# Optimization experiments

Measured on AMD Instinct MI355X. Metric: run time of the kernel, lower is better.

## Reference

```python
import jax, jax.numpy as jnp
import numpy as np

B, S, D, H = 4, 2048, 512, 8
DEPTH = D // H


def setup_inputs() -> dict:
    key = jax.random.key(0)
    ks = jax.random.split(key, 12)
    scale = 0.02
    inp = {
        "q": jax.random.normal(ks[0], (B, S, D), dtype=jnp.float32),
        "k": jax.random.normal(ks[1], (B, S, D), dtype=jnp.float32),
        "v": jax.random.normal(ks[2], (B, S, D), dtype=jnp.float32),
        "mask": jax.random.randint(ks[3], (B, S, S), 0, 2, dtype=jnp.int32),
        "wq": jax.random.normal(ks[4], (D, D), dtype=jnp.float32) * scale,
        "bq": jnp.zeros((D,), dtype=jnp.float32),
        "wk": jax.random.normal(ks[5], (D, D), dtype=jnp.float32) * scale,
        "bk": jnp.zeros((D,), dtype=jnp.float32),
        "wv": jax.random.normal(ks[6], (D, D), dtype=jnp.float32) * scale,
        "bv": jnp.zeros((D,), dtype=jnp.float32),
        "wo": jax.random.normal(ks[7], (D, D), dtype=jnp.float32) * scale,
        "bo": jnp.zeros((D,), dtype=jnp.float32),
    }
    return inp


def _split_heads(x):
    # [B, S, D] -> [B, H, S, depth]
    b, s, _ = x.shape
    return x.reshape(b, s, H, DEPTH).transpose(0, 2, 1, 3)


def reference(q, k, v, mask, wq, bq, wk, bk, wv, bv, wo, bo):
    qh = _split_heads(q @ wq + bq)
    kh = _split_heads(k @ wk + bk)
    vh = _split_heads(v @ wv + bv)
    # scaled dot-product attention with additive mask, materializing [B,H,S,S]
    scores = jnp.einsum("bhqd,bhkd->bhqk", qh, kh) / jnp.sqrt(
        jnp.asarray(DEPTH, jnp.float32)
    )
    scores = scores + mask[:, None, :, :].astype(jnp.float32) * (-1e9)
    w = jax.nn.softmax(scores, axis=-1)
    o = jnp.einsum("bhqk,bhkd->bhqd", w, vh)
    o = o.transpose(0, 2, 1, 3).reshape(q.shape[0], -1, D)  # [B, S, D]
    return o @ wo + bo
```

## Files before the change

kernel.cpp:

```cpp
#include <hip/hip_runtime.h>
#include <hip/hip_bf16.h>
#include <stdint.h>

#define B_ 4
#define S_ 2048
#define D_ 512
#define H_ 8

typedef __attribute__((ext_vector_type(8))) short short8;
typedef __attribute__((ext_vector_type(4))) short short4v;
typedef __attribute__((ext_vector_type(4))) float f32x4;
typedef __attribute__((ext_vector_type(4))) unsigned short u16x4;

#define MFMA16(a,b,c) __builtin_amdgcn_mfma_f32_16x16x32_bf16((a),(b),(c),0,0,0)

#if __has_builtin(__builtin_amdgcn_mfma_f32_16x16x16bf16_1k)
#define HAVE16K 1
#define MFMA16K(a,b,c) __builtin_amdgcn_mfma_f32_16x16x16bf16_1k((a),(b),(c),0,0,0)
#else
#define HAVE16K 0
#endif

#if __has_builtin(__builtin_amdgcn_sbfe)
#define SBFE1(v, off) ((uint32_t)__builtin_amdgcn_sbfe((int)(v), (off), 1))
#else
#define SBFE1(v, off) ((uint32_t)(((int32_t)((v) << (31-(off)))) >> 31))
#endif

__device__ __forceinline__ unsigned short f2bf(float f){
    return __builtin_bit_cast(unsigned short, __float2bfloat16(f));
}

__device__ __forceinline__ float maskf(float p, uint32_t keep){
    return __builtin_bit_cast(float, __builtin_bit_cast(uint32_t, p) & keep);
}

__device__ __forceinline__ float max3f(float a, float b, float c){
    float d;
    asm("v_max3_f32 %0, %1, %2, %3" : "=v"(d) : "v"(a), "v"(b), "v"(c));
    return d;
}

__device__ __forceinline__ void gload_lds16(const void* g, void* l){
    __builtin_amdgcn_global_load_lds((const __attribute__((address_space(1))) uint32_t*)g,
                                     (__attribute__((address_space(3))) uint32_t*)l, 16, 0, 0);
}

__global__ __launch_bounds__(256) void maskpack_kernel(const int* __restrict__ mask,
                                                       uint32_t* __restrict__ out)
{
    int idx = blockIdx.x*256 + threadIdx.x;
    const int4* p = (const int4*)(mask + (size_t)idx*32);
    uint32_t bits = 0;
    #pragma unroll
    for (int c=0;c<8;c++){
        int4 v = p[c];
        if (v.x) bits |= 1u << (c*4+0);
        if (v.y) bits |= 1u << (c*4+1);
        if (v.z) bits |= 1u << (c*4+2);
        if (v.w) bits |= 1u << (c*4+3);
    }
    out[idx] = bits;
}

__global__ __launch_bounds__(256) void wtrans_kernel(const float* __restrict__ wq,
                                                     const float* __restrict__ wk,
                                                     const float* __restrict__ wv,
                                                     const float* __restrict__ wo,
                                                     unsigned short* __restrict__ wt)
{
    int f = blockIdx.x*256 + threadIdx.x;
    int mat = f >> 18;
    int rem = f & 262143;
    const float* Wm = (mat==0)?wq:(mat==1)?wk:(mat==2)?wv:wo;
    int kk = rem >> 9, nn = rem & 511;
    wt[(size_t)mat*262144 + (size_t)nn*512 + kk] = f2bf(Wm[rem]);
}

__global__ __launch_bounds__(256) void proj_kernel(
    const float* __restrict__ q, const float* __restrict__ k, const float* __restrict__ v,
    const float* __restrict__ bq, const float* __restrict__ bk, const float* __restrict__ bv,
    const unsigned short* __restrict__ wt, unsigned short* __restrict__ outb)
{
    __shared__ uint8_t smem[16384];
    const int t = threadIdx.x, l = t&63, w = t>>6, g = l>>4, ln = l&15;
    const int z = blockIdx.z;
    const float* X = (z==0)? q : (z==1)? k : v;
    const float* bias = (z==0)? bq : (z==1)? bk : bv;
    const unsigned short* WTz = wt + (size_t)z*(D_*D_);
    unsigned short* out = outb + (size_t)z*((size_t)B_*H_*S_*64);
    const float scale = (z==0)? 0.18033688011112042f : 1.0f;
    const int m0 = blockIdx.x*128, n0 = blockIdx.y*128;
    uint8_t* As = smem; uint8_t* Bs = smem + 8192;
    const int RB = (w>>1)*64, CB = (w&1)*64;

    const f32x4 zz = {0.f,0.f,0.f,0.f};
    f32x4 acc[4][4];
    #pragma unroll
    for (int i=0;i<4;i++)
        #pragma unroll
        for (int j=0;j<4;j++) acc[i][j] = zz;

    for (int k0=0; k0<D_; k0+=32){
        __syncthreads();
        #pragma unroll
        for (int i=0;i<2;i++){
            int qc = w + i*4;
            int row = qc*16 + (l>>2);
            int colb = ((l&3)*16) ^ ((row&3)<<4);
            gload_lds16((const uint8_t*)WTz + (((size_t)(n0+row)*D_ + k0)<<1) + colb,
                        Bs + qc*1024);
        }
        #pragma unroll
        for (int i=0;i<2;i++){
            int c = t + i*256;
            int row = c>>2, cc = c&3;
            const float4* src = (const float4*)(X + (size_t)(m0+row)*D_ + k0 + cc*8);
            float4 u0 = src[0], u1 = src[1];
            uint32_t c0,c1,c2,c3;
            asm("v_cvt_pk_bf16_f32 %0, %1, %2" : "=v"(c0) : "v"(u0.x), "v"(u0.y));
            asm("v_cvt_pk_bf16_f32 %0, %1, %2" : "=v"(c1) : "v"(u0.z), "v"(u0.w));
            asm("v_cvt_pk_bf16_f32 %0, %1, %2" : "=v"(c2) : "v"(u1.x), "v"(u1.y));
            asm("v_cvt_pk_bf16_f32 %0, %1, %2" : "=v"(c3) : "v"(u1.z), "v"(u1.w));
            uint4 pk4; pk4.x=c0; pk4.y=c1; pk4.z=c2; pk4.w=c3;
            *(uint4*)(As + row*64 + ((cc*16) ^ ((row&3)<<4))) = pk4;
        }
        __syncthreads();
        short8 af[4], bfr[4];
        #pragma unroll
        for (int ai=0; ai<4; ai++){
            int row = RB + 16*ai + ln;
            af[ai] = *(const short8*)(As + row*64 + ((16*g) ^ ((row&3)<<4)));
        }
        #pragma unroll
        for (int bj=0; bj<4; bj++){
            int row = CB + 16*bj + ln;
            bfr[bj] = *(const short8*)(Bs + row*64 + ((16*g) ^ ((row&3)<<4)));
        }
        if (z == 2){
            #pragma unroll
            for (int ai=0; ai<4; ai++)
                #pragma unroll
                for (int bj=0; bj<4; bj++)
                    acc[ai][bj] = MFMA16(bfr[bj], af[ai], acc[ai][bj]);
        } else {
            #pragma unroll
            for (int ai=0; ai<4; ai++)
                #pragma unroll
                for (int bj=0; bj<4; bj++)
                    acc[ai][bj] = MFMA16(af[ai], bfr[bj], acc[ai][bj]);
        }
    }

    if (z == 2){
        #pragma unroll
        for (int bj=0; bj<4; bj++){
            #pragma unroll
            for (int ai=0; ai<4; ai++){
                int s = m0 + RB + 16*ai + ln;
                #pragma unroll
                for (int r=0;r<4;r++){
                    int gn = n0 + CB + 16*bj + 4*g + r;
                    float val = acc[ai][bj][r] + bias[gn];
                    out[((size_t)(s>>11)*D_ + gn)*S_ + (s&2047)] = f2bf(val);
                }
            }
        }
    } else {
        #pragma unroll
        for (int bj=0; bj<4; bj++){
            int gn = n0 + CB + 16*bj + ln;
            float bv2 = bias[gn];
            int h = gn >> 6, dep = gn & 63;
            #pragma unroll
            for (int ai=0; ai<4; ai++){
                #pragma unroll
                for (int r=0;r<4;r++){
                    int gm = m0 + RB + 16*ai + 4*g + r;
                    float val = (acc[ai][bj][r] + bv2) * scale;
                    size_t o = ((size_t)(gm>>11)*H_ + h)*((size_t)S_*64) + (size_t)(gm&2047)*64 + dep;
                    out[o] = f2bf(val);
                }
            }
        }
    }
}

__global__ __launch_bounds__(256, 4) void attn_kernel(
    const unsigned short* __restrict__ qb, const unsigned short* __restrict__ kb,
    const unsigned short* __restrict__ vtb, const uint32_t* __restrict__ mb,
    unsigned short* __restrict__ ao)
{
#if HAVE16K
    __shared__ uint8_t smem[32768];
#else
    __shared__ uint8_t smem[40960];
#endif
    const int t = threadIdx.x, l = t&63, w = t>>6, g = l>>4, ln = l&15;
    const int bh = blockIdx.y;
    const int b = bh >> 3;
    const int q0 = blockIdx.x * 64;
    const unsigned short* Q  = qb + (size_t)bh*((size_t)S_*64);
    const unsigned short* K  = kb + (size_t)bh*((size_t)S_*64);
    const unsigned short* VT = vtb + ((size_t)b*D_ + (bh&7)*64)*S_;

    const int qrow = q0 + 16*w + ln;
    const short8 qf0 = *(const short8*)(Q + (size_t)qrow*64 + 8*g);
    const short8 qf1 = *(const short8*)(Q + (size_t)qrow*64 + 8*g + 32);

    const int Msw = (ln&7)<<4;
    const int sw0 = (16*g) ^ Msw;
    const int sw1 = (16*g + 64) ^ Msw;
    uint8_t* kB0 = smem + ln*128 + sw0;
    uint8_t* kB1 = smem + ln*128 + sw1;
#if HAVE16K
    uint8_t* vB  = smem + 16384 + ln*128;
    const int vo0 = (8*g     ) ^ Msw;
    const int vo1 = (8*g + 32) ^ Msw;
    const int vo2 = (8*g + 64) ^ Msw;
    const int vo3 = (8*g + 96) ^ Msw;
#else
    uint8_t* Pw = smem + 32768 + w*2048;
    uint8_t* prd0 = Pw + ln*128 + sw0;
    uint8_t* prd1 = Pw + ln*128 + sw1;
#endif

    int krow0 = w*8 + (l>>3), krow1 = (w+4)*8 + (l>>3);
    int colb0 = ((l&7)*16) ^ ((krow0&7)<<4);
    int colb1 = ((l&7)*16) ^ ((krow1&7)<<4);
    int kof0 = krow0*128 + colb0,     kof1 = krow1*128 + colb1;
    int vof0 = krow0*(S_*2) + colb0,  vof1 = krow1*(S_*2) + colb1;
    const int ldo0 = w*1024, ldo1 = (w+4)*1024;

    const uint2* mptr = (const uint2*)(mb + ((size_t)b*S_ + qrow)*64);

    const f32x4 zz = {0.f,0.f,0.f,0.f};
    f32x4 O[4], O5 = zz;
    #pragma unroll
    for (int i=0;i<4;i++) O[i] = zz;
    float c = 0.f;

    const short4v onesv = {0x3F80,0x3F80,0x3F80,0x3F80};
#if !HAVE16K
    const short8 ones8 = {0x3F80,0x3F80,0x3F80,0x3F80,0x3F80,0x3F80,0x3F80,0x3F80};
#endif

    gload_lds16((const uint8_t*)K  + kof0, smem + ldo0);
    gload_lds16((const uint8_t*)K  + kof1, smem + ldo1);
    gload_lds16((const uint8_t*)VT + vof0, smem + 16384 + ldo0);
    gload_lds16((const uint8_t*)VT + vof1, smem + 16384 + ldo1);
    kof0 += 8192; kof1 += 8192; vof0 += 128; vof1 += 128;
    int curb = 0;
    uint2 mmc = mptr[0];

    for (int it=0; it<S_/64; ++it){
        __syncthreads();
        if (it < S_/64 - 1){
            int nx = curb ^ 8192;
            gload_lds16((const uint8_t*)K  + kof0, smem + nx + ldo0);
            gload_lds16((const uint8_t*)K  + kof1, smem + nx + ldo1);
            gload_lds16((const uint8_t*)VT + vof0, smem + 16384 + nx + ldo0);
            gload_lds16((const uint8_t*)VT + vof1, smem + 16384 + nx + ldo1);
            kof0 += 8192; kof1 += 8192; vof0 += 128; vof1 += 128;
        }
        uint2 mmn = mptr[(it+1)&31];
        const uint8_t* b0 = kB0 + curb;
        const uint8_t* b1 = kB1 + curb;

        f32x4 st[4];
        __builtin_amdgcn_s_setprio(1);
        #pragma unroll
        for (int t4=0;t4<4;t4++){
            short8 kf0 = *(const short8*)(b0 + 2048*t4);
            short8 kf1 = *(const short8*)(b1 + 2048*t4);
            st[t4] = MFMA16(kf0, qf0, zz);
            st[t4] = MFMA16(kf1, qf1, st[t4]);
        }
        __builtin_amdgcn_s_setprio(0);

        float m0a = max3f(st[0][0], st[0][1], st[0][2]);
        float m1a = max3f(st[0][3], st[1][0], st[1][1]);
        float m2a = max3f(st[1][2], st[1][3], st[2][0]);
        float m3a = max3f(st[2][1], st[2][2], st[2][3]);
        float m4a = max3f(st[3][0], st[3][1], st[3][2]);
        float lmax = fmaxf(max3f(m0a, m1a, m2a), max3f(m3a, m4a, st[3][3]));
        if (__builtin_expect(__any(lmax > c + 8.0f), 0)){
            float rm = lmax;
            rm = fmaxf(rm, __shfl_xor(rm, 16));
            rm = fmaxf(rm, __shfl_xor(rm, 32));
            float cnew = fmaxf(c, rm);
            float al = __builtin_amdgcn_exp2f(c - cnew);
            c = cnew;
            #pragma unroll
            for (int r=0;r<4;r++){
                float aO = __shfl(al, 4*g + r);
                #pragma unroll
                for (int db=0; db<4; db++) O[db][r] *= aO;
                O5[r] *= aO;
            }
        }

        uint32_t mi0 = (~mmc.x) >> (4*g);
        uint32_t mi1 = (~mmc.y) >> (4*g);
        short4v pa[4];
        auto genp = [&](float cc){
            #pragma unroll
            for (int t4=0;t4<4;t4++){
                uint32_t mi = (t4 >= 2) ? mi1 : mi0;
                const int base = (t4&1)*16;
                float p0 = maskf(__builtin_amdgcn_exp2f(st[t4][0] - cc), SBFE1(mi, base+0));
                float p1 = maskf(__builtin_amdgcn_exp2f(st[t4][1] - cc), SBFE1(mi, base+1));
                float p2 = maskf(__builtin_amdgcn_exp2f(st[t4][2] - cc), SBFE1(mi, base+2));
                float p3 = maskf(__builtin_amdgcn_exp2f(st[t4][3] - cc), SBFE1(mi, base+3));
                uint32_t lo, hi;
                asm("v_cvt_pk_bf16_f32 %0, %1, %2" : "=v"(lo) : "v"(p0), "v"(p1));
                asm("v_cvt_pk_bf16_f32 %0, %1, %2" : "=v"(hi) : "v"(p2), "v"(p3));
                uint2 u; u.x = lo; u.y = hi;
                pa[t4] = __builtin_bit_cast(short4v, u);
            }
        };
        if (__builtin_expect(__all(c == 0.0f), 1)) genp(0.0f); else genp(c);
        mmc = mmn;

#if HAVE16K
        __builtin_amdgcn_s_setprio(1);
        const uint8_t* vb = vB + curb;
        #pragma unroll
        for (int db=0; db<4; db++){
            short4v vf0 = *(const short4v*)(vb + 2048*db + vo0);
            short4v vf1 = *(const short4v*)(vb + 2048*db + vo1);
            short4v vf2 = *(const short4v*)(vb + 2048*db + vo2);
            short4v vf3 = *(const short4v*)(vb + 2048*db + vo3);
            O[db] = MFMA16K(pa[0], vf0, O[db]);
            O[db] = MFMA16K(pa[1], vf1, O[db]);
            O[db] = MFMA16K(pa[2], vf2, O[db]);
            O[db] = MFMA16K(pa[3], vf3, O[db]);
        }
        O5 = MFMA16K(pa[0], onesv, O5);
        O5 = MFMA16K(pa[1], onesv, O5);
        O5 = MFMA16K(pa[2], onesv, O5);
        O5 = MFMA16K(pa[3], onesv, O5);
        __builtin_amdgcn_s_setprio(0);
#else
        #pragma unroll
        for (int t4=0;t4<4;t4++){
            uint2 u = __builtin_bit_cast(uint2, pa[t4]);
            *(uint2*)(Pw + ln*128 + ((32*t4 + 8*g) ^ Msw)) = u;
        }
        asm volatile("s_waitcnt lgkmcnt(0)" ::: "memory");
        short8 pa0 = *(const short8*)prd0;
        short8 pa1 = *(const short8*)prd1;
        __builtin_amdgcn_s_setprio(1);
        #pragma unroll
        for (int db=0; db<4; db++){
            int dr = 16*db + ln;
            short8 vf0 = *(const short8*)(smem + 16384 + curb + dr*128 + ((16*g     ) ^ ((dr&7)<<4)));
            short8 vf1 = *(const short8*)(smem + 16384 + curb + dr*128 + ((16*g + 64) ^ ((dr&7)<<4)));
            O[db] = MFMA16(pa0, vf0, O[db]);
            O[db] = MFMA16(pa1, vf1, O[db]);
        }
        O5 = MFMA16(pa0, ones8, O5);
        O5 = MFMA16(pa1, ones8, O5);
        __builtin_amdgcn_s_setprio(0);
#endif
        curb ^= 8192;
    }

    #pragma unroll
    for (int r=0;r<4;r++){
        float inv = 1.0f / O5[r];
        int gm = b*S_ + q0 + 16*w + 4*g + r;
        #pragma unroll
        for (int db=0; db<4; db++){
            int col = (bh&7)*64 + 16*db + ln;
            ao[(size_t)gm*D_ + col] = f2bf(O[db][r]*inv);
        }
    }
}

__global__ __launch_bounds__(256) void outproj_kernel(
    const unsigned short* __restrict__ ao, const unsigned short* __restrict__ wt,
    const float* __restrict__ bo, float* __restrict__ out)
{
    __shared__ uint8_t smem[16384];
    const int t = threadIdx.x, l = t&63, w = t>>6, g = l>>4, ln = l&15;
    const unsigned short* WTz = wt + (size_t)3*(D_*D_);
    const int m0 = blockIdx.x*128, n0 = blockIdx.y*128;
    uint8_t* As = smem; uint8_t* Bs = smem + 8192;
    const int RB = (w>>1)*64, CB = (w&1)*64;

    const f32x4 zz = {0.f,0.f,0.f,0.f};
    f32x4 acc[4][4];
    #pragma unroll
    for (int i=0;i<4;i++)
        #pragma unroll
        for (int j=0;j<4;j++) acc[i][j] = zz;

    for (int k0=0; k0<D_; k0+=32){
        __syncthreads();
        #pragma unroll
        for (int i=0;i<2;i++){
            int qc = w + i*4;
            int row = qc*16 + (l>>2);
            int colb = ((l&3)*16) ^ ((row&3)<<4);
            gload_lds16((const uint8_t*)WTz + (((size_t)(n0+row)*D_ + k0)<<1) + colb,
                        Bs + qc*1024);
            gload_lds16((const uint8_t*)ao + (((size_t)(m0+row)*D_ + k0)<<1) + colb,
                        As + qc*1024);
        }
        __syncthreads();
        short8 af[4], bfr[4];
        #pragma unroll
        for (int ai=0; ai<4; ai++){
            int row = RB + 16*ai + ln;
            af[ai] = *(const short8*)(As + row*64 + ((16*g) ^ ((row&3)<<4)));
        }
        #pragma unroll
        for (int bj=0; bj<4; bj++){
            int row = CB + 16*bj + ln;
            bfr[bj] = *(const short8*)(Bs + row*64 + ((16*g) ^ ((row&3)<<4)));
        }
        #pragma unroll
        for (int ai=0; ai<4; ai++)
            #pragma unroll
            for (int bj=0; bj<4; bj++)
                acc[ai][bj] = MFMA16(af[ai], bfr[bj], acc[ai][bj]);
    }

    #pragma unroll
    for (int bj=0; bj<4; bj++){
        int gn = n0 + CB + 16*bj + ln;
        float bv2 = bo[gn];
        #pragma unroll
        for (int ai=0; ai<4; ai++){
            #pragma unroll
            for (int r=0;r<4;r++){
                int gm = m0 + RB + 16*ai + 4*g + r;
                out[(size_t)gm*D_ + gn] = acc[ai][bj][r] + bv2;
            }
        }
    }
}

extern "C" void kernel_launch(void* const* d_in, const int* in_sizes, int n_in,
                              void* d_out, int out_size, void* d_ws, size_t ws_size,
                              hipStream_t stream)
{
    const float* q  = (const float*)d_in[0];
    const float* k  = (const float*)d_in[1];
    const float* v  = (const float*)d_in[2];
    const int* mask = (const int*)d_in[3];
    const float* wq = (const float*)d_in[4];
    const float* bq = (const float*)d_in[5];
    const float* wk = (const float*)d_in[6];
    const float* bk = (const float*)d_in[7];
    const float* wv = (const float*)d_in[8];
    const float* bv = (const float*)d_in[9];
    const float* wo = (const float*)d_in[10];
    const float* bo = (const float*)d_in[11];

    uint8_t* ws = (uint8_t*)d_ws;
    unsigned short* qkvb = (unsigned short*)ws;
    unsigned short* ao   = (unsigned short*)(ws + 25165824);
    unsigned short* wt   = (unsigned short*)(ws + 33554432);
    uint32_t*       mb   = (uint32_t*)      (ws + 35651584);
    float* out = (float*)d_out;

    maskpack_kernel<<<dim3(2048), dim3(256), 0, stream>>>(mask, mb);
    wtrans_kernel<<<dim3(4096), dim3(256), 0, stream>>>(wq, wk, wv, wo, wt);
    proj_kernel<<<dim3(64,4,3), dim3(256), 0, stream>>>(q, k, v, bq, bk, bv, wt, qkvb);
    attn_kernel<<<dim3(32,32), dim3(256), 0, stream>>>(qkvb, qkvb + 4194304, qkvb + 8388608, mb, ao);
    outproj_kernel<<<dim3(64,4), dim3(256), 0, stream>>>(ao, wt, bo, out);
}
```

Baseline: 135.0 us.

## Merge prep kernels, widen GEMM K-tile to 64, remap attention blocks

Combines the mask-packing and weight-transpose kernels into one launch to save a kernel launch. Doubles the K step of the projection and output-projection GEMMs to 64 with an 8-way XOR swizzle, which halves the number of barrier-separated iterations at the cost of twice the shared memory. Remaps the attention grid so that consecutive blocks cover different heads of the same query tile, which changes the order in which mask and K/V data are reused through cache.

```diff
diff --git a/kernel.cpp b/kernel.cpp
--- a/kernel.cpp
+++ b/kernel.cpp
@@ -46,35 +46,34 @@
                                      (__attribute__((address_space(3))) uint32_t*)l, 16, 0, 0);
 }
 
-__global__ __launch_bounds__(256) void maskpack_kernel(const int* __restrict__ mask,
-                                                       uint32_t* __restrict__ out)
+__global__ __launch_bounds__(256) void prep_kernel(
+    const int* __restrict__ mask, uint32_t* __restrict__ mout,
+    const float* __restrict__ wq, const float* __restrict__ wk,
+    const float* __restrict__ wv, const float* __restrict__ wo,
+    unsigned short* __restrict__ wt)
 {
-    int idx = blockIdx.x*256 + threadIdx.x;
-    const int4* p = (const int4*)(mask + (size_t)idx*32);
-    uint32_t bits = 0;
-    #pragma unroll
-    for (int c=0;c<8;c++){
-        int4 v = p[c];
-        if (v.x) bits |= 1u << (c*4+0);
-        if (v.y) bits |= 1u << (c*4+1);
-        if (v.z) bits |= 1u << (c*4+2);
-        if (v.w) bits |= 1u << (c*4+3);
-    }
-    out[idx] = bits;
-}
-
-__global__ __launch_bounds__(256) void wtrans_kernel(const float* __restrict__ wq,
-                                                     const float* __restrict__ wk,
-                                                     const float* __restrict__ wv,
-                                                     const float* __restrict__ wo,
-                                                     unsigned short* __restrict__ wt)
-{
-    int f = blockIdx.x*256 + threadIdx.x;
-    int mat = f >> 18;
-    int rem = f & 262143;
-    const float* Wm = (mat==0)?wq:(mat==1)?wk:(mat==2)?wv:wo;
-    int kk = rem >> 9, nn = rem & 511;
-    wt[(size_t)mat*262144 + (size_t)nn*512 + kk] = f2bf(Wm[rem]);
+    int bid = blockIdx.x;
+    if (bid < 4096){
+        int f = bid*256 + threadIdx.x;
+        int mat = f >> 18;
+        int rem = f & 262143;
+        const float* Wm = (mat==0)?wq:(mat==1)?wk:(mat==2)?wv:wo;
+        int kk = rem >> 9, nn = rem & 511;
+        wt[(size_t)mat*262144 + (size_t)nn*512 + kk] = f2bf(Wm[rem]);
+    } else {
+        int idx = (bid-4096)*256 + threadIdx.x;
+        const int4* p = (const int4*)(mask + (size_t)idx*32);
+        uint32_t bits = 0;
+        #pragma unroll
+        for (int c=0;c<8;c++){
+            int4 v = p[c];
+            if (v.x) bits |= 1u << (c*4+0);
+            if (v.y) bits |= 1u << (c*4+1);
+            if (v.z) bits |= 1u << (c*4+2);
+            if (v.w) bits |= 1u << (c*4+3);
+        }
+        mout[idx] = bits;
+    }
 }
 
 __global__ __launch_bounds__(256) void proj_kernel(
@@ -82,7 +81,7 @@
     const float* __restrict__ bq, const float* __restrict__ bk, const float* __restrict__ bv,
     const unsigned short* __restrict__ wt, unsigned short* __restrict__ outb)
 {
-    __shared__ uint8_t smem[16384];
+    __shared__ uint8_t smem[32768];
     const int t = threadIdx.x, l = t&63, w = t>>6, g = l>>4, ln = l&15;
     const int z = blockIdx.z;
     const float* X = (z==0)? q : (z==1)? k : v;
@@ -91,7 +90,7 @@
     unsigned short* out = outb + (size_t)z*((size_t)B_*H_*S_*64);
     const float scale = (z==0)? 0.18033688011112042f : 1.0f;
     const int m0 = blockIdx.x*128, n0 = blockIdx.y*128;
-    uint8_t* As = smem; uint8_t* Bs = smem + 8192;
+    uint8_t* As = smem; uint8_t* Bs = smem + 16384;
     const int RB = (w>>1)*64, CB = (w&1)*64;
 
     const f32x4 zz = {0.f,0.f,0.f,0.f};
@@ -101,20 +100,20 @@
         #pragma unroll
         for (int j=0;j<4;j++) acc[i][j] = zz;
 
-    for (int k0=0; k0<D_; k0+=32){
+    for (int k0=0; k0<D_; k0+=64){
         __syncthreads();
         #pragma unroll
-        for (int i=0;i<2;i++){
+        for (int i=0;i<4;i++){
             int qc = w + i*4;
-            int row = qc*16 + (l>>2);
-            int colb = ((l&3)*16) ^ ((row&3)<<4);
+            int row = qc*8 + (l>>3);
+            int colb = ((l&7)*16) ^ ((row&7)<<4);
             gload_lds16((const uint8_t*)WTz + (((size_t)(n0+row)*D_ + k0)<<1) + colb,
                         Bs + qc*1024);
         }
         #pragma unroll
-        for (int i=0;i<2;i++){
+        for (int i=0;i<4;i++){
             int c = t + i*256;
-            int row = c>>2, cc = c&3;
+            int row = c>>3, cc = c&7;
             const float4* src = (const float4*)(X + (size_t)(m0+row)*D_ + k0 + cc*8);
             float4 u0 = src[0], u1 = src[1];
             uint32_t c0,c1,c2,c3;
@@ -123,32 +122,35 @@
             asm("v_cvt_pk_bf16_f32 %0, %1, %2" : "=v"(c2) : "v"(u1.x), "v"(u1.y));
             asm("v_cvt_pk_bf16_f32 %0, %1, %2" : "=v"(c3) : "v"(u1.z), "v"(u1.w));
             uint4 pk4; pk4.x=c0; pk4.y=c1; pk4.z=c2; pk4.w=c3;
-            *(uint4*)(As + row*64 + ((cc*16) ^ ((row&3)<<4))) = pk4;
+            *(uint4*)(As + row*128 + ((cc*16) ^ ((row&7)<<4))) = pk4;
         }
         __syncthreads();
-        short8 af[4], bfr[4];
-        #pragma unroll
-        for (int ai=0; ai<4; ai++){
-            int row = RB + 16*ai + ln;
-            af[ai] = *(const short8*)(As + row*64 + ((16*g) ^ ((row&3)<<4)));
-        }
-        #pragma unroll
-        for (int bj=0; bj<4; bj++){
-            int row = CB + 16*bj + ln;
-            bfr[bj] = *(const short8*)(Bs + row*64 + ((16*g) ^ ((row&3)<<4)));
-        }
-        if (z == 2){
-            #pragma unroll
-            for (int ai=0; ai<4; ai++)
-                #pragma unroll
-                for (int bj=0; bj<4; bj++)
-                    acc[ai][bj] = MFMA16(bfr[bj], af[ai], acc[ai][bj]);
-        } else {
-            #pragma unroll
-            for (int ai=0; ai<4; ai++)
-                #pragma unroll
-                for (int bj=0; bj<4; bj++)
-                    acc[ai][bj] = MFMA16(af[ai], bfr[bj], acc[ai][bj]);
+        #pragma unroll
+        for (int kc=0; kc<2; kc++){
+            short8 af[4], bfr[4];
+            #pragma unroll
+            for (int ai=0; ai<4; ai++){
+                int row = RB + 16*ai + ln;
+                af[ai] = *(const short8*)(As + row*128 + ((16*g + 64*kc) ^ ((row&7)<<4)));
+            }
+            #pragma unroll
+            for (int bj=0; bj<4; bj++){
+                int row = CB + 16*bj + ln;
+                bfr[bj] = *(const short8*)(Bs + row*128 + ((16*g + 64*kc) ^ ((row&7)<<4)));
+            }
+            if (z == 2){
+                #pragma unroll
+                for (int ai=0; ai<4; ai++)
+                    #pragma unroll
+                    for (int bj=0; bj<4; bj++)
+                        acc[ai][bj] = MFMA16(bfr[bj], af[ai], acc[ai][bj]);
+            } else {
+                #pragma unroll
+                for (int ai=0; ai<4; ai++)
+                    #pragma unroll
+                    for (int bj=0; bj<4; bj++)
+                        acc[ai][bj] = MFMA16(af[ai], bfr[bj], acc[ai][bj]);
+            }
         }
     }
 
@@ -197,9 +199,11 @@
     __shared__ uint8_t smem[40960];
 #endif
     const int t = threadIdx.x, l = t&63, w = t>>6, g = l>>4, ln = l&15;
-    const int bh = blockIdx.y;
+    const int fid = blockIdx.x + 32*blockIdx.y;
+    const int slot = fid >> 3;
+    const int bh = (fid & 7) + 8*(slot >> 5);
+    const int q0 = (slot & 31) * 64;
     const int b = bh >> 3;
-    const int q0 = blockIdx.x * 64;
     const unsigned short* Q  = qb + (size_t)bh*((size_t)S_*64);
     const unsigned short* K  = kb + (size_t)bh*((size_t)S_*64);
     const unsigned short* VT = vtb + ((size_t)b*D_ + (bh&7)*64)*S_;
@@ -382,11 +386,11 @@
     const unsigned short* __restrict__ ao, const unsigned short* __restrict__ wt,
     const float* __restrict__ bo, float* __restrict__ out)
 {
-    __shared__ uint8_t smem[16384];
+    __shared__ uint8_t smem[32768];
     const int t = threadIdx.x, l = t&63, w = t>>6, g = l>>4, ln = l&15;
     const unsigned short* WTz = wt + (size_t)3*(D_*D_);
     const int m0 = blockIdx.x*128, n0 = blockIdx.y*128;
-    uint8_t* As = smem; uint8_t* Bs = smem + 8192;
+    uint8_t* As = smem; uint8_t* Bs = smem + 16384;
     const int RB = (w>>1)*64, CB = (w&1)*64;
 
     const f32x4 zz = {0.f,0.f,0.f,0.f};
@@ -396,35 +400,38 @@
         #pragma unroll
         for (int j=0;j<4;j++) acc[i][j] = zz;
 
-    for (int k0=0; k0<D_; k0+=32){
+    for (int k0=0; k0<D_; k0+=64){
         __syncthreads();
         #pragma unroll
-        for (int i=0;i<2;i++){
+        for (int i=0;i<4;i++){
             int qc = w + i*4;
-            int row = qc*16 + (l>>2);
-            int colb = ((l&3)*16) ^ ((row&3)<<4);
+            int row = qc*8 + (l>>3);
+            int colb = ((l&7)*16) ^ ((row&7)<<4);
             gload_lds16((const uint8_t*)WTz + (((size_t)(n0+row)*D_ + k0)<<1) + colb,
                         Bs + qc*1024);
             gload_lds16((const uint8_t*)ao + (((size_t)(m0+row)*D_ + k0)<<1) + colb,
                         As + qc*1024);
         }
         __syncthreads();
-        short8 af[4], bfr[4];
-        #pragma unroll
-        for (int ai=0; ai<4; ai++){
-            int row = RB + 16*ai + ln;
-            af[ai] = *(const short8*)(As + row*64 + ((16*g) ^ ((row&3)<<4)));
-        }
-        #pragma unroll
-        for (int bj=0; bj<4; bj++){
-            int row = CB + 16*bj + ln;
-            bfr[bj] = *(const short8*)(Bs + row*64 + ((16*g) ^ ((row&3)<<4)));
-        }
-        #pragma unroll
-        for (int ai=0; ai<4; ai++)
-            #pragma unroll
-            for (int bj=0; bj<4; bj++)
-                acc[ai][bj] = MFMA16(af[ai], bfr[bj], acc[ai][bj]);
+        #pragma unroll
+        for (int kc=0; kc<2; kc++){
+            short8 af[4], bfr[4];
+            #pragma unroll
+            for (int ai=0; ai<4; ai++){
+                int row = RB + 16*ai + ln;
+                af[ai] = *(const short8*)(As + row*128 + ((16*g + 64*kc) ^ ((row&7)<<4)));
+            }
+            #pragma unroll
+            for (int bj=0; bj<4; bj++){
+                int row = CB + 16*bj + ln;
+                bfr[bj] = *(const short8*)(Bs + row*128 + ((16*g + 64*kc) ^ ((row&7)<<4)));
+            }
+            #pragma unroll
+            for (int ai=0; ai<4; ai++)
+                #pragma unroll
+                for (int bj=0; bj<4; bj++)
+                    acc[ai][bj] = MFMA16(af[ai], bfr[bj], acc[ai][bj]);
+        }
     }
 
     #pragma unroll
@@ -466,8 +473,7 @@
     uint32_t*       mb   = (uint32_t*)      (ws + 35651584);
     float* out = (float*)d_out;
 
-    maskpack_kernel<<<dim3(2048), dim3(256), 0, stream>>>(mask, mb);
-    wtrans_kernel<<<dim3(4096), dim3(256), 0, stream>>>(wq, wk, wv, wo, wt);
+    prep_kernel<<<dim3(6144), dim3(256), 0, stream>>>(mask, mb, wq, wk, wv, wo, wt);
     proj_kernel<<<dim3(64,4,3), dim3(256), 0, stream>>>(q, k, v, bq, bk, bv, wt, qkvb);
     attn_kernel<<<dim3(32,32), dim3(256), 0, stream>>>(qkvb, qkvb + 4194304, qkvb + 8388608, mb, ao);
     outproj_kernel<<<dim3(64,4), dim3(256), 0, stream>>>(ao, wt, bo, out);
```

Measured after the change: 123.8 us. 8.3% less time.
